# Kernel tuning notes

Hardware: AMD Instinct MI355X
Metric: run time of the kernel (lower is better)

The kernel has to match this reference:

```python
import jax, jax.numpy as jnp
import numpy as np

N = 100000
E = 1600000
HEADS = 4
OUT_C = 32
IN_C = 128
NEG_SLOPE = 0.2
EPS = 1e-16


def setup_inputs() -> dict:
    key = jax.random.key(0)
    ks = jax.random.split(key, 6)
    x = jax.random.normal(ks[0], (N, IN_C), dtype=jnp.float32)
    edge_index = jax.random.randint(ks[1], (2, E), 0, N, dtype=jnp.int32)
    # Glorot-ish scaled params (scale only affects magnitudes, not the math)
    W = jax.random.normal(ks[2], (IN_C, HEADS * OUT_C), dtype=jnp.float32) * (1.0 / np.sqrt(IN_C))
    att_src = jax.random.normal(ks[3], (HEADS, OUT_C), dtype=jnp.float32) * (1.0 / np.sqrt(OUT_C))
    att_dst = jax.random.normal(ks[4], (HEADS, OUT_C), dtype=jnp.float32) * (1.0 / np.sqrt(OUT_C))
    bias = jnp.zeros((HEADS * OUT_C,), dtype=jnp.float32)
    return {"x": x, "edge_index": edge_index, "W": W, "att_src": att_src, "att_dst": att_dst, "bias": bias}


def reference(x, edge_index, W, att_src, att_dst, bias):
    n = x.shape[0]
    heads, out_c = att_src.shape
    # add self loops (PyG add_self_loops=True): append edges (i, i)
    loop = jnp.arange(n, dtype=edge_index.dtype)
    src = jnp.concatenate([edge_index[0], loop])  # source j
    dst = jnp.concatenate([edge_index[1], loop])  # target i

    # linear projection: [n, heads, out_c]
    h = (x @ W).reshape(n, heads, out_c)

    # per-node attention logits: [n, heads]
    a_src = jnp.einsum('nhc,hc->nh', h, att_src)
    a_dst = jnp.einsum('nhc,hc->nh', h, att_dst)

    # per-edge score with LeakyReLU: [e, heads]
    e = a_src[src] + a_dst[dst]
    e = jnp.where(e >= 0, e, NEG_SLOPE * e)

    # segment softmax over incoming edges per target node
    m = jax.ops.segment_max(e, dst, num_segments=n)          # [n, heads]
    m = jnp.where(jnp.isfinite(m), m, 0.0)                   # nodes with no in-edges
    ex = jnp.exp(e - m[dst])
    s = jax.ops.segment_sum(ex, dst, num_segments=n)         # [n, heads]
    alpha = ex / (s[dst] + EPS)                              # [e, heads]

    # weighted scatter-aggregate of source features
    msg = h[src] * alpha[:, :, None]                         # [e, heads, out_c]
    out = jax.ops.segment_sum(msg, dst, num_segments=n)      # [n, heads, out_c]
    return out.reshape(n, heads * out_c) + bias
```

## Files before the change

kernel.cpp:

```cpp
#include <hip/hip_runtime.h>
#include <hip/hip_fp16.h>

#define NEG_SLOPE 0.2f
#define EPS 1e-16f
#define MAXNB 512
#define BSHIFT 8
#define BNODES 256
#define CHUNK 8192
#define CAPR 6144
#define CAPC 8192
#define GB 512

typedef _Float16 f16x8 __attribute__((ext_vector_type(8)));
typedef float    f32x4 __attribute__((ext_vector_type(4)));

__global__ __launch_bounds__(256) void gemm_mfma(const float* __restrict__ x,
                                                 const float* __restrict__ W,
                                                 const float* __restrict__ att_src,
                                                 const float* __restrict__ att_dst,
                                                 __half* __restrict__ h16,
                                                 float* __restrict__ a_src,
                                                 float* __restrict__ a_dst, int N) {
    __shared__ _Float16 ldsT[4][16][264];
    __shared__ float atts[4][33];
    __shared__ float attd[4][33];
    for (int i = threadIdx.x; i < 128; i += 256) {
        atts[i >> 5][i & 31] = att_src[i];
        attd[i >> 5][i & 31] = att_dst[i];
    }
    __syncthreads();
    const int lane = threadIdx.x & 63;
    const int wid  = threadIdx.x >> 6;
    const int q    = lane >> 4;
    const int t    = lane & 15;
    f16x8 bfrag[8][4];
#pragma unroll
    for (int ct = 0; ct < 8; ++ct)
#pragma unroll
        for (int kt = 0; kt < 4; ++kt) {
            const float* wp = W + (size_t)(kt * 32 + q * 8) * 128 + ct * 16 + t;
            f16x8 b;
#pragma unroll
            for (int j = 0; j < 8; ++j) b[j] = (_Float16)wp[(size_t)j * 128];
            bfrag[ct][kt] = b;
        }
    const int lrow = lane >> 2;
    const int lhd  = lane & 3;
    const int strips = (N + 15) >> 4;
    for (int s = blockIdx.x * 4 + wid; s < strips; s += GB * 4) {
        int row0 = s << 4;
        int row  = row0 + t;
        const float* xp = x + (size_t)((row < N) ? row : (N - 1)) * 128;
        f16x8 afrag[4];
#pragma unroll
        for (int kt = 0; kt < 4; ++kt) {
            float4 u0 = *(const float4*)(xp + kt * 32 + q * 8);
            float4 u1 = *(const float4*)(xp + kt * 32 + q * 8 + 4);
            f16x8 a;
            a[0] = (_Float16)u0.x; a[1] = (_Float16)u0.y;
            a[2] = (_Float16)u0.z; a[3] = (_Float16)u0.w;
            a[4] = (_Float16)u1.x; a[5] = (_Float16)u1.y;
            a[6] = (_Float16)u1.z; a[7] = (_Float16)u1.w;
            afrag[kt] = a;
        }
        f32x4 acc[8];
#pragma unroll
        for (int ct = 0; ct < 8; ++ct) acc[ct] = (f32x4){0.f, 0.f, 0.f, 0.f};
#pragma unroll
        for (int kt = 0; kt < 4; ++kt)
#pragma unroll
            for (int ct = 0; ct < 8; ++ct)
                acc[ct] = __builtin_amdgcn_mfma_f32_16x16x32_f16(afrag[kt], bfrag[ct][kt],
                                                                 acc[ct], 0, 0, 0);
#pragma unroll
        for (int ct = 0; ct < 8; ++ct)
#pragma unroll
            for (int r = 0; r < 4; ++r)
                ldsT[wid][q * 4 + r][ct * 16 + t] = (_Float16)acc[ct][r];
        float4 raw[4];
#pragma unroll
        for (int j = 0; j < 4; ++j)
            raw[j] = *(const float4*)&ldsT[wid][lrow][lhd * 32 + j * 8];
        int orow = row0 + lrow;
        if (orow < N) {
            float4* gp = (float4*)(h16 + (size_t)orow * 128 + lhd * 32);
            gp[0] = raw[0]; gp[1] = raw[1]; gp[2] = raw[2]; gp[3] = raw[3];
            const __half2* hv = (const __half2*)raw;
            float s1 = 0.f, s2 = 0.f;
#pragma unroll
            for (int c = 0; c < 16; ++c) {
                float2 f = __half22float2(hv[c]);
                s1 = fmaf(f.x, atts[lhd][2 * c], s1);
                s1 = fmaf(f.y, atts[lhd][2 * c + 1], s1);
                s2 = fmaf(f.x, attd[lhd][2 * c], s2);
                s2 = fmaf(f.y, attd[lhd][2 * c + 1], s2);
            }
            a_src[orow * 4 + lhd] = s1;
            a_dst[orow * 4 + lhd] = s2;
        }
    }
}

__global__ __launch_bounds__(256) void binA(const int* __restrict__ ei,
                                            int* __restrict__ gcursor,
                                            unsigned* __restrict__ records,
                                            int E, int N) {
    __shared__ unsigned stage[CHUNK];
    __shared__ unsigned short bkt[CHUNK];
    __shared__ int lhist[MAXNB];
    __shared__ int lbase[MAXNB];
    int T = E + N;
    int c0 = blockIdx.x * CHUNK;
    for (int i = threadIdx.x; i < MAXNB; i += 256) lhist[i] = 0;
    __syncthreads();
    int cnt = min(CHUNK, T - c0);
    for (int i = threadIdx.x; i < cnt; i += 256) {
        int e = c0 + i;
        int src, dst;
        if (e < E) { src = ei[e]; dst = ei[E + e]; }
        else       { src = dst = e - E; }
        int b = dst >> BSHIFT;
        stage[i] = ((unsigned)(dst & (BNODES - 1)) << 17) | (unsigned)src;
        bkt[i]   = (unsigned short)b;
        atomicAdd(&lhist[b], 1);
    }
    __syncthreads();
    for (int b = threadIdx.x; b < MAXNB; b += 256) {
        int h = lhist[b];
        lbase[b] = h ? (b * CAPR + atomicAdd(&gcursor[b], h)) : 0;
    }
    __syncthreads();
    for (int i = threadIdx.x; i < cnt; i += 256) {
        int b = bkt[i];
        int pos = atomicAdd(&lbase[b], 1);
        records[pos] = stage[i];
    }
}

__global__ __launch_bounds__(256) void binB(const unsigned* __restrict__ records,
                                            const int* __restrict__ gcursor,
                                            int* __restrict__ counts,
                                            int* __restrict__ offs,
                                            int* __restrict__ csr, int N) {
    __shared__ int lcsr[CAPC];
    __shared__ int ncnt[BNODES];
    __shared__ int relcur[BNODES];
    __shared__ int psum[256];
    int b = blockIdx.x;
    int node0 = b << BSHIFT;
    int nn = min(BNODES, N - node0);
    int t = threadIdx.x;
    ncnt[t] = 0;
    __syncthreads();
    int rbase = b * CAPR;
    int cbase = b * CAPC;
    int cntb  = gcursor[b];
    for (int r = t; r < cntb; r += 256)
        atomicAdd(&ncnt[records[rbase + r] >> 17], 1);
    __syncthreads();
    int va  = ncnt[t];
    int vap = (va + 7) & ~7;
    psum[t] = vap;
    __syncthreads();
    for (int off = 1; off < 256; off <<= 1) {
        int y = (t >= off) ? psum[t - off] : 0;
        __syncthreads();
        psum[t] += y;
        __syncthreads();
    }
    int ptot = psum[255];
    int ex = psum[t] - vap;
    relcur[t] = ex;
    if (t < nn) { offs[node0 + t] = cbase + ex; counts[node0 + t] = va; }
    __syncthreads();
    for (int r = t; r < cntb; r += 256) {
        unsigned rec = records[rbase + r];
        int pos = atomicAdd(&relcur[rec >> 17], 1);
        lcsr[pos] = rec & 0x1FFFF;
    }
    __syncthreads();
    for (int r = t; r < ptot; r += 256)
        csr[cbase + r] = lcsr[r];
}

__global__ __launch_bounds__(256) void aggr_csr(const int* __restrict__ csr,
                                                const int* __restrict__ offs,
                                                const int* __restrict__ counts,
                                                const float* __restrict__ a_src,
                                                const float* __restrict__ a_dst,
                                                const __half* __restrict__ h16,
                                                const float* __restrict__ bias,
                                                float* __restrict__ out, int N) {
    int node = blockIdx.x * 16 + (threadIdx.x >> 4);
    if (node >= N) return;
    int lane = threadIdx.x & 15;
    int hd   = lane >> 2;
    int c0   = lane * 8;
    float ad = a_dst[node * 4 + hd];
    int beg  = offs[node];
    int cnt  = counts[node];
    float acc[8];
#pragma unroll
    for (int j = 0; j < 8; ++j) acc[j] = 0.f;
    float den = 0.f;
    int k = 0;
    for (; k + 4 <= cnt; k += 4) {
        int b = beg + k;
        int s0 = csr[b], s1 = csr[b + 1], s2 = csr[b + 2], s3 = csr[b + 3];
        float e0 = a_src[s0 * 4 + hd];
        float e1 = a_src[s1 * 4 + hd];
        float e2 = a_src[s2 * 4 + hd];
        float e3 = a_src[s3 * 4 + hd];
        float4 g0 = *(const float4*)(h16 + (size_t)s0 * 128 + c0);
        float4 g1 = *(const float4*)(h16 + (size_t)s1 * 128 + c0);
        float4 g2 = *(const float4*)(h16 + (size_t)s2 * 128 + c0);
        float4 g3 = *(const float4*)(h16 + (size_t)s3 * 128 + c0);
        float sc;
        sc = e0 + ad; sc = (sc >= 0.f) ? sc : NEG_SLOPE * sc; float w0 = __expf(sc);
        sc = e1 + ad; sc = (sc >= 0.f) ? sc : NEG_SLOPE * sc; float w1 = __expf(sc);
        sc = e2 + ad; sc = (sc >= 0.f) ? sc : NEG_SLOPE * sc; float w2 = __expf(sc);
        sc = e3 + ad; sc = (sc >= 0.f) ? sc : NEG_SLOPE * sc; float w3 = __expf(sc);
        den += w0 + w1 + w2 + w3;
        const __half2* p0 = (const __half2*)&g0;
        const __half2* p1 = (const __half2*)&g1;
        const __half2* p2 = (const __half2*)&g2;
        const __half2* p3 = (const __half2*)&g3;
#pragma unroll
        for (int j = 0; j < 4; ++j) {
            float2 f0 = __half22float2(p0[j]);
            float2 f1 = __half22float2(p1[j]);
            float2 f2 = __half22float2(p2[j]);
            float2 f3 = __half22float2(p3[j]);
            acc[2 * j]     = fmaf(w0, f0.x, acc[2 * j]);
            acc[2 * j + 1] = fmaf(w0, f0.y, acc[2 * j + 1]);
            acc[2 * j]     = fmaf(w1, f1.x, acc[2 * j]);
            acc[2 * j + 1] = fmaf(w1, f1.y, acc[2 * j + 1]);
            acc[2 * j]     = fmaf(w2, f2.x, acc[2 * j]);
            acc[2 * j + 1] = fmaf(w2, f2.y, acc[2 * j + 1]);
            acc[2 * j]     = fmaf(w3, f3.x, acc[2 * j]);
            acc[2 * j + 1] = fmaf(w3, f3.y, acc[2 * j + 1]);
        }
    }
    for (; k < cnt; ++k) {
        int b = beg + k;
        int s = csr[b];
        float e0 = a_src[s * 4 + hd];
        float4 g = *(const float4*)(h16 + (size_t)s * 128 + c0);
        float sc = e0 + ad; sc = (sc >= 0.f) ? sc : NEG_SLOPE * sc;
        float w = __expf(sc);
        den += w;
        const __half2* p = (const __half2*)&g;
#pragma unroll
        for (int j = 0; j < 4; ++j) {
            float2 f = __half22float2(p[j]);
            acc[2 * j]     = fmaf(w, f.x, acc[2 * j]);
            acc[2 * j + 1] = fmaf(w, f.y, acc[2 * j + 1]);
        }
    }
    float inv = 1.f / (den + EPS);
    float4 o0, o1;
    o0.x = fmaf(acc[0], inv, bias[c0]);
    o0.y = fmaf(acc[1], inv, bias[c0 + 1]);
    o0.z = fmaf(acc[2], inv, bias[c0 + 2]);
    o0.w = fmaf(acc[3], inv, bias[c0 + 3]);
    o1.x = fmaf(acc[4], inv, bias[c0 + 4]);
    o1.y = fmaf(acc[5], inv, bias[c0 + 5]);
    o1.z = fmaf(acc[6], inv, bias[c0 + 6]);
    o1.w = fmaf(acc[7], inv, bias[c0 + 7]);
    float* op = out + (size_t)node * 128 + c0;
    *(float4*)op       = o0;
    *(float4*)(op + 4) = o1;
}

extern "C" void kernel_launch(void* const* d_in, const int* in_sizes, int n_in,
                              void* d_out, int out_size, void* d_ws, size_t ws_size,
                              hipStream_t stream) {
    const float* x       = (const float*)d_in[0];
    const int*   ei      = (const int*)  d_in[1];
    const float* W       = (const float*)d_in[2];
    const float* att_src = (const float*)d_in[3];
    const float* att_dst = (const float*)d_in[4];
    const float* bias    = (const float*)d_in[5];
    float*       out     = (float*)d_out;

    const int N  = in_sizes[0] / 128;
    const int E  = in_sizes[1] / 2;
    const int T  = E + N;
    const int NB = (N + BNODES - 1) >> BSHIFT;

    __half*   h16     = (__half*)d_ws;
    float*    a_src   = (float*)(h16 + (size_t)N * 128);
    float*    a_dst   = a_src + (size_t)N * 4;
    int*      counts  = (int*)(a_dst + (size_t)N * 4);
    int*      offs    = counts + N;
    int*      gcursor = offs + N;
    int*      csr     = gcursor + MAXNB;
    unsigned* records = (unsigned*)(csr + (size_t)NB * CAPC);

    (void)hipMemsetAsync(gcursor, 0, MAXNB * sizeof(int), stream);

    gemm_mfma<<<GB, 256, 0, stream>>>(x, W, att_src, att_dst, h16, a_src, a_dst, N);

    binA<<<(T + CHUNK - 1) / CHUNK, 256, 0, stream>>>(ei, gcursor, records, E, N);
    binB<<<NB, 256, 0, stream>>>(records, gcursor, counts, offs, csr, N);

    aggr_csr<<<(N + 15) / 16, 256, 0, stream>>>(csr, offs, counts, a_src, a_dst, h16, bias, out, N);
}
```

Before: 238.5 us.

## Fuse per-bucket CSR build into aggregation kernel using LDS-resident edge lists

Merges binB and aggr_csr into one kernel. Each 512-thread block builds the CSR for its 256-node bucket in LDS and then aggregates those nodes directly, reading source indices from LDS. This removes the global csr/offs/counts write and re-read and one kernel launch. In exchange, only 391 blocks are launched, each looping over 8 passes of 32 nodes, which cuts parallelism and may leave CUs idle or unbalanced during the gather-heavy phase.

```diff
diff --git a/kernel.cpp b/kernel.cpp
--- a/kernel.cpp
+++ b/kernel.cpp
@@ -137,139 +137,133 @@
     }
 }
 
-__global__ __launch_bounds__(256) void binB(const unsigned* __restrict__ records,
-                                            const int* __restrict__ gcursor,
-                                            int* __restrict__ counts,
-                                            int* __restrict__ offs,
-                                            int* __restrict__ csr, int N) {
+__global__ __launch_bounds__(512, 8) void aggr_fused(const unsigned* __restrict__ records,
+                                                     const int* __restrict__ gcursor,
+                                                     const float* __restrict__ a_src,
+                                                     const float* __restrict__ a_dst,
+                                                     const __half* __restrict__ h16,
+                                                     const float* __restrict__ bias,
+                                                     float* __restrict__ out, int N) {
     __shared__ int lcsr[CAPC];
     __shared__ int ncnt[BNODES];
+    __shared__ int nbeg[BNODES];
     __shared__ int relcur[BNODES];
-    __shared__ int psum[256];
+    __shared__ int psum[BNODES];
     int b = blockIdx.x;
     int node0 = b << BSHIFT;
     int nn = min(BNODES, N - node0);
     int t = threadIdx.x;
-    ncnt[t] = 0;
+    if (t < BNODES) ncnt[t] = 0;
     __syncthreads();
     int rbase = b * CAPR;
-    int cbase = b * CAPC;
     int cntb  = gcursor[b];
-    for (int r = t; r < cntb; r += 256)
+    for (int r = t; r < cntb; r += 512)
         atomicAdd(&ncnt[records[rbase + r] >> 17], 1);
     __syncthreads();
-    int va  = ncnt[t];
-    int vap = (va + 7) & ~7;
-    psum[t] = vap;
-    __syncthreads();
-    for (int off = 1; off < 256; off <<= 1) {
-        int y = (t >= off) ? psum[t - off] : 0;
+    int va = 0, vap = 0;
+    if (t < BNODES) { va = ncnt[t]; vap = (va + 7) & ~7; psum[t] = vap; }
+    __syncthreads();
+    for (int off = 1; off < BNODES; off <<= 1) {
+        int y = 0;
+        if (t < BNODES && t >= off) y = psum[t - off];
         __syncthreads();
-        psum[t] += y;
+        if (t < BNODES) psum[t] += y;
         __syncthreads();
     }
-    int ptot = psum[255];
-    int ex = psum[t] - vap;
-    relcur[t] = ex;
-    if (t < nn) { offs[node0 + t] = cbase + ex; counts[node0 + t] = va; }
-    __syncthreads();
-    for (int r = t; r < cntb; r += 256) {
+    if (t < BNODES) {
+        int ex = psum[t] - vap;
+        nbeg[t]   = ex;
+        relcur[t] = ex;
+    }
+    __syncthreads();
+    for (int r = t; r < cntb; r += 512) {
         unsigned rec = records[rbase + r];
         int pos = atomicAdd(&relcur[rec >> 17], 1);
         lcsr[pos] = rec & 0x1FFFF;
     }
     __syncthreads();
-    for (int r = t; r < ptot; r += 256)
-        csr[cbase + r] = lcsr[r];
-}
-
-__global__ __launch_bounds__(256) void aggr_csr(const int* __restrict__ csr,
-                                                const int* __restrict__ offs,
-                                                const int* __restrict__ counts,
-                                                const float* __restrict__ a_src,
-                                                const float* __restrict__ a_dst,
-                                                const __half* __restrict__ h16,
-                                                const float* __restrict__ bias,
-                                                float* __restrict__ out, int N) {
-    int node = blockIdx.x * 16 + (threadIdx.x >> 4);
-    if (node >= N) return;
-    int lane = threadIdx.x & 15;
+    int lane = t & 15;
+    int ln   = t >> 4;
     int hd   = lane >> 2;
     int c0   = lane * 8;
-    float ad = a_dst[node * 4 + hd];
-    int beg  = offs[node];
-    int cnt  = counts[node];
-    float acc[8];
-#pragma unroll
-    for (int j = 0; j < 8; ++j) acc[j] = 0.f;
-    float den = 0.f;
-    int k = 0;
-    for (; k + 4 <= cnt; k += 4) {
-        int b = beg + k;
-        int s0 = csr[b], s1 = csr[b + 1], s2 = csr[b + 2], s3 = csr[b + 3];
-        float e0 = a_src[s0 * 4 + hd];
-        float e1 = a_src[s1 * 4 + hd];
-        float e2 = a_src[s2 * 4 + hd];
-        float e3 = a_src[s3 * 4 + hd];
-        float4 g0 = *(const float4*)(h16 + (size_t)s0 * 128 + c0);
-        float4 g1 = *(const float4*)(h16 + (size_t)s1 * 128 + c0);
-        float4 g2 = *(const float4*)(h16 + (size_t)s2 * 128 + c0);
-        float4 g3 = *(const float4*)(h16 + (size_t)s3 * 128 + c0);
-        float sc;
-        sc = e0 + ad; sc = (sc >= 0.f) ? sc : NEG_SLOPE * sc; float w0 = __expf(sc);
-        sc = e1 + ad; sc = (sc >= 0.f) ? sc : NEG_SLOPE * sc; float w1 = __expf(sc);
-        sc = e2 + ad; sc = (sc >= 0.f) ? sc : NEG_SLOPE * sc; float w2 = __expf(sc);
-        sc = e3 + ad; sc = (sc >= 0.f) ? sc : NEG_SLOPE * sc; float w3 = __expf(sc);
-        den += w0 + w1 + w2 + w3;
-        const __half2* p0 = (const __half2*)&g0;
-        const __half2* p1 = (const __half2*)&g1;
-        const __half2* p2 = (const __half2*)&g2;
-        const __half2* p3 = (const __half2*)&g3;
-#pragma unroll
-        for (int j = 0; j < 4; ++j) {
-            float2 f0 = __half22float2(p0[j]);
-            float2 f1 = __half22float2(p1[j]);
-            float2 f2 = __half22float2(p2[j]);
-            float2 f3 = __half22float2(p3[j]);
-            acc[2 * j]     = fmaf(w0, f0.x, acc[2 * j]);
-            acc[2 * j + 1] = fmaf(w0, f0.y, acc[2 * j + 1]);
-            acc[2 * j]     = fmaf(w1, f1.x, acc[2 * j]);
-            acc[2 * j + 1] = fmaf(w1, f1.y, acc[2 * j + 1]);
-            acc[2 * j]     = fmaf(w2, f2.x, acc[2 * j]);
-            acc[2 * j + 1] = fmaf(w2, f2.y, acc[2 * j + 1]);
-            acc[2 * j]     = fmaf(w3, f3.x, acc[2 * j]);
-            acc[2 * j + 1] = fmaf(w3, f3.y, acc[2 * j + 1]);
-        }
-    }
-    for (; k < cnt; ++k) {
-        int b = beg + k;
-        int s = csr[b];
-        float e0 = a_src[s * 4 + hd];
-        float4 g = *(const float4*)(h16 + (size_t)s * 128 + c0);
-        float sc = e0 + ad; sc = (sc >= 0.f) ? sc : NEG_SLOPE * sc;
-        float w = __expf(sc);
-        den += w;
-        const __half2* p = (const __half2*)&g;
-#pragma unroll
-        for (int j = 0; j < 4; ++j) {
-            float2 f = __half22float2(p[j]);
-            acc[2 * j]     = fmaf(w, f.x, acc[2 * j]);
-            acc[2 * j + 1] = fmaf(w, f.y, acc[2 * j + 1]);
-        }
-    }
-    float inv = 1.f / (den + EPS);
-    float4 o0, o1;
-    o0.x = fmaf(acc[0], inv, bias[c0]);
-    o0.y = fmaf(acc[1], inv, bias[c0 + 1]);
-    o0.z = fmaf(acc[2], inv, bias[c0 + 2]);
-    o0.w = fmaf(acc[3], inv, bias[c0 + 3]);
-    o1.x = fmaf(acc[4], inv, bias[c0 + 4]);
-    o1.y = fmaf(acc[5], inv, bias[c0 + 5]);
-    o1.z = fmaf(acc[6], inv, bias[c0 + 6]);
-    o1.w = fmaf(acc[7], inv, bias[c0 + 7]);
-    float* op = out + (size_t)node * 128 + c0;
-    *(float4*)op       = o0;
-    *(float4*)(op + 4) = o1;
+    for (int pass = 0; pass < BNODES / 32; ++pass) {
+        int nl = pass * 32 + ln;
+        if (nl >= nn) continue;
+        int node = node0 + nl;
+        float ad = a_dst[node * 4 + hd];
+        int beg  = nbeg[nl];
+        int cnt  = ncnt[nl];
+        float acc[8];
+#pragma unroll
+        for (int j = 0; j < 8; ++j) acc[j] = 0.f;
+        float den = 0.f;
+        int k = 0;
+        for (; k + 4 <= cnt; k += 4) {
+            int bb = beg + k;
+            int s0 = lcsr[bb], s1 = lcsr[bb + 1], s2 = lcsr[bb + 2], s3 = lcsr[bb + 3];
+            float e0 = a_src[s0 * 4 + hd];
+            float e1 = a_src[s1 * 4 + hd];
+            float e2 = a_src[s2 * 4 + hd];
+            float e3 = a_src[s3 * 4 + hd];
+            float4 g0 = *(const float4*)(h16 + (size_t)s0 * 128 + c0);
+            float4 g1 = *(const float4*)(h16 + (size_t)s1 * 128 + c0);
+            float4 g2 = *(const float4*)(h16 + (size_t)s2 * 128 + c0);
+            float4 g3 = *(const float4*)(h16 + (size_t)s3 * 128 + c0);
+            float sc;
+            sc = e0 + ad; sc = (sc >= 0.f) ? sc : NEG_SLOPE * sc; float w0 = __expf(sc);
+            sc = e1 + ad; sc = (sc >= 0.f) ? sc : NEG_SLOPE * sc; float w1 = __expf(sc);
+            sc = e2 + ad; sc = (sc >= 0.f) ? sc : NEG_SLOPE * sc; float w2 = __expf(sc);
+            sc = e3 + ad; sc = (sc >= 0.f) ? sc : NEG_SLOPE * sc; float w3 = __expf(sc);
+            den += w0 + w1 + w2 + w3;
+            const __half2* p0 = (const __half2*)&g0;
+            const __half2* p1 = (const __half2*)&g1;
+            const __half2* p2 = (const __half2*)&g2;
+            const __half2* p3 = (const __half2*)&g3;
+#pragma unroll
+            for (int j = 0; j < 4; ++j) {
+                float2 f0 = __half22float2(p0[j]);
+                float2 f1 = __half22float2(p1[j]);
+                float2 f2 = __half22float2(p2[j]);
+                float2 f3 = __half22float2(p3[j]);
+                acc[2 * j]     = fmaf(w0, f0.x, acc[2 * j]);
+                acc[2 * j + 1] = fmaf(w0, f0.y, acc[2 * j + 1]);
+                acc[2 * j]     = fmaf(w1, f1.x, acc[2 * j]);
+                acc[2 * j + 1] = fmaf(w1, f1.y, acc[2 * j + 1]);
+                acc[2 * j]     = fmaf(w2, f2.x, acc[2 * j]);
+                acc[2 * j + 1] = fmaf(w2, f2.y, acc[2 * j + 1]);
+                acc[2 * j]     = fmaf(w3, f3.x, acc[2 * j]);
+                acc[2 * j + 1] = fmaf(w3, f3.y, acc[2 * j + 1]);
+            }
+        }
+        for (; k < cnt; ++k) {
+            int s = lcsr[beg + k];
+            float e0 = a_src[s * 4 + hd];
+            float4 g = *(const float4*)(h16 + (size_t)s * 128 + c0);
+            float sc = e0 + ad; sc = (sc >= 0.f) ? sc : NEG_SLOPE * sc;
+            float w = __expf(sc);
+            den += w;
+            const __half2* p = (const __half2*)&g;
+#pragma unroll
+            for (int j = 0; j < 4; ++j) {
+                float2 f = __half22float2(p[j]);
+                acc[2 * j]     = fmaf(w, f.x, acc[2 * j]);
+                acc[2 * j + 1] = fmaf(w, f.y, acc[2 * j + 1]);
+            }
+        }
+        float inv = 1.f / (den + EPS);
+        float4 o0, o1;
+        o0.x = fmaf(acc[0], inv, bias[c0]);
+        o0.y = fmaf(acc[1], inv, bias[c0 + 1]);
+        o0.z = fmaf(acc[2], inv, bias[c0 + 2]);
+        o0.w = fmaf(acc[3], inv, bias[c0 + 3]);
+        o1.x = fmaf(acc[4], inv, bias[c0 + 4]);
+        o1.y = fmaf(acc[5], inv, bias[c0 + 5]);
+        o1.z = fmaf(acc[6], inv, bias[c0 + 6]);
+        o1.w = fmaf(acc[7], inv, bias[c0 + 7]);
+        float* op = out + (size_t)node * 128 + c0;
+        *(float4*)op       = o0;
+        *(float4*)(op + 4) = o1;
+    }
 }
 
 extern "C" void kernel_launch(void* const* d_in, const int* in_sizes, int n_in,
@@ -291,18 +285,14 @@
     __half*   h16     = (__half*)d_ws;
     float*    a_src   = (float*)(h16 + (size_t)N * 128);
     float*    a_dst   = a_src + (size_t)N * 4;
-    int*      counts  = (int*)(a_dst + (size_t)N * 4);
-    int*      offs    = counts + N;
-    int*      gcursor = offs + N;
-    int*      csr     = gcursor + MAXNB;
-    unsigned* records = (unsigned*)(csr + (size_t)NB * CAPC);
+    int*      gcursor = (int*)(a_dst + (size_t)N * 4);
+    unsigned* records = (unsigned*)(gcursor + MAXNB);
 
     (void)hipMemsetAsync(gcursor, 0, MAXNB * sizeof(int), stream);
 
     gemm_mfma<<<GB, 256, 0, stream>>>(x, W, att_src, att_dst, h16, a_src, a_dst, N);
 
     binA<<<(T + CHUNK - 1) / CHUNK, 256, 0, stream>>>(ei, gcursor, records, E, N);
-    binB<<<NB, 256, 0, stream>>>(records, gcursor, counts, offs, csr, N);
-
-    aggr_csr<<<(N + 15) / 16, 256, 0, stream>>>(csr, offs, counts, a_src, a_dst, h16, bias, out, N);
-}
+
+    aggr_fused<<<NB, 512, 0, stream>>>(records, gcursor, a_src, a_dst, h16, bias, out, N);
+}
```

Result: faster. 230.4 us (median of 2 runs) (-3.4%).
